# Performance work log

Measured on AMD Instinct MI355X. Metric: run time of the kernel, lower is better.

The kernel has to match this reference:

```python
import math
import jax, jax.numpy as jnp
import numpy as np

N_LAYERS = 2
D = 256        # d_input
N = 32         # d_state
BATCH = 8
L = 2048
SPK = 2


def setup_inputs() -> dict:
    key = jax.random.key(0)
    ks = jax.random.split(key, 20)
    def rn(i, shape, s=1.0):
        return jax.random.normal(ks[i], shape, jnp.float32) * s
    w = 0.02  # weight init scale
    lo, hi = math.log(1e-3), math.log(1e-1)
    return dict(
        x=rn(0, (BATCH, D, L)),
        ln_g=jnp.ones((N_LAYERS, 2, D), jnp.float32),
        ln_b=jnp.zeros((N_LAYERS, 2, D), jnp.float32),
        log_dt=lo + jax.random.uniform(ks[1], (N_LAYERS, D), jnp.float32) * (hi - lo),
        A_log_re=rn(2, (N_LAYERS, D, N), 0.5),
        A_im=rn(3, (N_LAYERS, D, N)) * math.pi,
        B_re=rn(4, (N_LAYERS, D, N), 0.5),
        B_im=rn(5, (N_LAYERS, D, N), 0.5),
        C_re=rn(6, (N_LAYERS, D, N), 0.5),
        C_im=rn(7, (N_LAYERS, D, N), 0.5),
        Dp=rn(8, (N_LAYERS, D)),
        s4o_W=rn(9, (N_LAYERS, D, D), w), s4o_b=jnp.zeros((N_LAYERS, D), jnp.float32),
        lin1_W=rn(10, (N_LAYERS, D, D), w), lin1_b=jnp.zeros((N_LAYERS, D), jnp.float32),
        lin2_W=rn(11, (N_LAYERS, D, D), w), lin2_b=jnp.zeros((N_LAYERS, D), jnp.float32),
        out_W0=rn(12, (D, D), w), out_b0=jnp.zeros((D,), jnp.float32),
        proj_W0=rn(13, (D, D), w), proj_b0=jnp.zeros((D,), jnp.float32),
        out_W1=rn(14, (D, SPK * D), w), out_b1=jnp.zeros((SPK * D,), jnp.float32),
        proj_W1=rn(15, (D, SPK * D), w), proj_b1=jnp.zeros((SPK * D,), jnp.float32),
    )


def _layernorm(x, g, b, eps=1e-5):
    m = jnp.mean(x, axis=-1, keepdims=True)
    v = jnp.var(x, axis=-1, keepdims=True)
    return (x - m) * jax.lax.rsqrt(v + eps) * g + b


def _s4(u, log_dt, A_log_re, A_im, B_re, B_im, C_re, C_im, Dp, oW, ob):
    # u: [B, L, H]. Diagonal SSM (ZOH discretization) -> global FFT convolution.
    Lq = u.shape[1]
    dt = jnp.exp(log_dt)                       # [H]
    A = -jnp.exp(A_log_re) + 1j * A_im         # [H, N], Re(A) < 0 for stability
    dtA = dt[:, None] * A                      # [H, N]
    dB = (B_re + 1j * B_im) * (jnp.exp(dtA) - 1.0) / A
    CB = (C_re + 1j * C_im) * dB               # [H, N]
    steps = jnp.arange(Lq)
    # Vandermonde kernel K[h, l] = 2 Re sum_n CB[h,n] * exp(dtA[h,n] * l)
    K = 2.0 * jnp.einsum('hn,hnl->hl', CB, jnp.exp(dtA[:, :, None] * steps)).real
    n = 2 * Lq  # linear (non-circular) convolution
    Uf = jnp.fft.rfft(u, n=n, axis=1)          # [B, nf, H]
    Kf = jnp.fft.rfft(K, n=n, axis=-1)         # [H, nf]
    y = jnp.fft.irfft(Uf * Kf.T[None], n=n, axis=1)[:, :Lq]
    y = y + u * Dp                              # skip connection D*u
    y = jax.nn.gelu(y, approximate=False)       # S4 activation='gelu'
    return y @ oW + ob                          # output_linear (postact='id')


def reference(x, ln_g, ln_b, log_dt, A_log_re, A_im, B_re, B_im, C_re, C_im, Dp,
              s4o_W, s4o_b, lin1_W, lin1_b, lin2_W, lin2_b,
              out_W0, out_b0, proj_W0, proj_b0, out_W1, out_b1, proj_W1, proj_b1):
    o = jnp.moveaxis(x, -1, -2)  # [B, L, D]
    heads = [(out_W0, out_b0, proj_W0, proj_b0), (out_W1, out_b1, proj_W1, proj_b1)]
    for i in range(N_LAYERS):
        oW, ob, pW, pb = heads[i]
        u = o
        o1 = _layernorm(u, ln_g[i, 0], ln_b[i, 0])
        o1 = _s4(o1, log_dt[i], A_log_re[i], A_im[i], B_re[i], B_im[i],
                 C_re[i], C_im[i], Dp[i], s4o_W[i], s4o_b[i])
        o1 = o1 @ lin1_W[i] + lin1_b[i] + u     # residual add
        o2 = _layernorm(o1, ln_g[i, 1], ln_b[i, 1])
        o2 = jax.nn.gelu(o2 @ lin2_W[i] + lin2_b[i], approximate=False)
        o = o2 @ oW + ob + (o1 @ pW + pb)
    o = jax.nn.relu(o)                          # output_activation
    Bsz, Lq, C = o.shape
    d = C // SPK
    o = jnp.moveaxis(o, -1, 0).reshape(SPK, d, Bsz, Lq)
    return jnp.moveaxis(o, 1, -2)               # [num_spks, B, d_input, L]
```

## Files before the change

kernel.cpp:

```cpp
#include <hip/hip_runtime.h>


#define BSZ 8
#define DM 256
#define LSEQ 2048
#define NST 32
#define TC 64
#define NCH 32
#define TOK (BSZ*LSEQ)
#define NL 2

typedef __attribute__((ext_vector_type(8))) short bf16x8;
typedef __attribute__((ext_vector_type(4))) float f32x4;
typedef unsigned short ushort_t;

__device__ __forceinline__ float b2f(unsigned short v) {
    unsigned int u = ((unsigned int)v) << 16;
    float f;
    __builtin_memcpy(&f, &u, 4);
    return f;
}
__device__ __forceinline__ unsigned short f2b(float f) {
    unsigned int u;
    __builtin_memcpy(&u, &f, 4);
    unsigned int r = (u + 0x7FFFu + ((u >> 16) & 1u)) >> 16;
    return (unsigned short)r;
}
__device__ __forceinline__ float gelu_f(float z) {
    float x = z * 0.70710678118654752f;
    float ax = fabsf(x);
    float t = 1.0f / (1.0f + 0.3275911f * ax);
    float poly = t * (0.254829592f + t * (-0.284496736f + t * (1.421413741f +
                 t * (-1.453152027f + t * 1.061405429f))));
    float erfax = 1.0f - poly * expf(-ax * ax);
    float er = (x < 0.0f) ? -erfax : erfax;
    return 0.5f * z * (1.0f + er);
}

__global__ void k_setup_modes(const float* log_dt, const float* Alr, const float* Aim,
                              const float* Bre, const float* Bim,
                              const float* Cre, const float* Cim,
                              float2* dtA, float2* lam, float2* lamT, float2* CB) {
    int idx = blockIdx.x * blockDim.x + threadIdx.x;
    if (idx >= NL * DM * NST) return;
    int h = (idx >> 5) & (DM - 1);
    int i = idx >> 13;
    float dt  = expf(log_dt[i * DM + h]);
    float Are = -expf(Alr[idx]);
    float Ai  = Aim[idx];
    float dr = dt * Are, di = dt * Ai;
    float er = expf(dr);
    float lr = er * cosf(di), li = er * sinf(di);
    float inv = 1.0f / (Are * Are + Ai * Ai);
    float e1r = lr - 1.0f, e1i = li;
    float tr = (e1r * Are + e1i * Ai) * inv;
    float ti = (e1i * Are - e1r * Ai) * inv;
    float br = Bre[idx], bi = Bim[idx];
    float dBr = br * tr - bi * ti, dBi = br * ti + bi * tr;
    float cr = Cre[idx], ci = Cim[idx];
    dtA[idx] = make_float2(dr, di);
    lam[idx] = make_float2(lr, li);
    CB[idx]  = make_float2(cr * dBr - ci * dBi, cr * dBi + ci * dBr);
    float pr = lr, pi = li;
    for (int s = 0; s < 6; ++s) { float nr = pr * pr - pi * pi; pi = 2.f * pr * pi; pr = nr; }
    lamT[idx] = make_float2(pr, pi);
}

__global__ void k_wcvt(const float* src, ushort_t* dst, int N) {
    int idx = blockIdx.x * 256 + threadIdx.x;
    if (idx >= N * 256) return;
    int n = idx >> 8, k = idx & 255;
    dst[idx] = f2b(src[(size_t)k * N + n]);
}

__global__ void k_wc_fuse(const float* Wa, const float* Wb, ushort_t* WBc) {
    int c = blockIdx.x;
    int r = threadIdx.x;
    const float* ar = Wa + (size_t)r * 256;
    float s = 0.f;
    for (int k = 0; k < 256; ++k) s = fmaf(ar[k], Wb[(size_t)k * 256 + c], s);
    WBc[(size_t)c * 256 + r] = f2b(s);
}
__global__ void k_bc_fuse(const float* s4ob, const float* Wb, const float* lin1b,
                          float* bc) {
    int c = threadIdx.x;
    float s = lin1b[c];
    for (int k = 0; k < 256; ++k) s = fmaf(s4ob[k], Wb[(size_t)k * 256 + c], s);
    bc[c] = s;
}

__global__ void k_setup_wk(const float2* dtA_l, const float2* lam_l, const float2* CB_l,
                           float* Ktab, float2* Wtab) {
    int idx = blockIdx.x * blockDim.x + threadIdx.x;
    if (idx >= DM * TC) return;
    int t = idx & (TC - 1);
    int h = idx >> 6;
    int base = h * NST;
    float ft = (float)t;
    float Ks = 0.f;
    for (int n = 0; n < NST; ++n) {
        float2 d = dtA_l[base + n]; float2 l1 = lam_l[base + n]; float2 cb = CB_l[base + n];
        float er = expf(d.x * ft);
        float cs = cosf(d.y * ft), sn = sinf(d.y * ft);
        float ltr = er * cs, lti = er * sn;
        Ks += cb.x * ltr - cb.y * lti;
        float p1r = ltr * l1.x - lti * l1.y, p1i = ltr * l1.y + lti * l1.x;
        Wtab[(h * NST + n) * TC + t] =
            make_float2(cb.x * p1r - cb.y * p1i, cb.x * p1i + cb.y * p1r);
    }
    Ktab[idx] = 2.f * Ks;
}

__global__ void k_transpose_in(const float* x, ushort_t* o) {
    __shared__ float tile[32][33];
    int b = blockIdx.z;
    int l0 = blockIdx.x * 32, d0 = blockIdx.y * 32;
    int tx = threadIdx.x, ty = threadIdx.y;
    for (int k = 0; k < 4; ++k)
        tile[ty + 8 * k][tx] = x[((size_t)b * DM + d0 + ty + 8 * k) * LSEQ + l0 + tx];
    __syncthreads();
    for (int k = 0; k < 4; ++k)
        o[((size_t)b * LSEQ + l0 + ty + 8 * k) * DM + d0 + tx] = f2b(tile[tx][ty + 8 * k]);
}

__global__ void k_layernorm(const ushort_t* src, ushort_t* dst,
                            const float* g, const float* bb) {
    __shared__ float r1[DM];
    __shared__ float r2[DM];
    int tok = blockIdx.x;
    int d = threadIdx.x;
    float v = b2f(src[(size_t)tok * DM + d]);
    r1[d] = v;
    r2[d] = v * v;
    __syncthreads();
    for (int s = DM / 2; s > 0; s >>= 1) {
        if (d < s) { r1[d] += r1[d + s]; r2[d] += r2[d + s]; }
        __syncthreads();
    }
    float m = r1[0] * (1.0f / DM);
    float var = r2[0] * (1.0f / DM) - m * m;
    float inv = rsqrtf(var + 1e-5f);
    dst[(size_t)tok * DM + d] = f2b((v - m) * inv * g[d] + bb[d]);
}

__global__ void k_layernorm_T(const ushort_t* src, ushort_t* dstT,
                              const float* g, const float* bb) {
    __shared__ float r1[DM];
    __shared__ float r2[DM];
    int tok = blockIdx.x;
    int d = threadIdx.x;
    float v = b2f(src[(size_t)tok * DM + d]);
    r1[d] = v;
    r2[d] = v * v;
    __syncthreads();
    for (int s = DM / 2; s > 0; s >>= 1) {
        if (d < s) { r1[d] += r1[d + s]; r2[d] += r2[d + s]; }
        __syncthreads();
    }
    float m = r1[0] * (1.0f / DM);
    float var = r2[0] * (1.0f / DM) - m * m;
    float inv = rsqrtf(var + 1e-5f);
    int b = tok >> 11, l = tok & 2047;
    dstT[((size_t)b * DM + d) * LSEQ + l] = f2b((v - m) * inv * g[d] + bb[d]);
}

__global__ void k_chunk_states(const ushort_t* uT, const float2* lam_l, float2* P) {
    int n = threadIdx.x & 31, hs = threadIdx.x >> 5;
    int c = blockIdx.x, h = blockIdx.y * 8 + hs, b = blockIdx.z;
    float2 lm = lam_l[h * NST + n];
    float sr = 0.f, si = 0.f;
    const ushort_t* up = uT + ((size_t)b * DM + h) * LSEQ + c * TC;
#pragma unroll 8
    for (int t = 0; t < TC; ++t) {
        float u = b2f(up[t]);
        float nr = fmaf(lm.x, sr, fmaf(-lm.y, si, u));
        float ni = fmaf(lm.x, si, lm.y * sr);
        sr = nr; si = ni;
    }
    P[(((size_t)b * DM + h) * NCH + c) * NST + n] = make_float2(sr, si);
}

__global__ void k_chunk_scan(const float2* lamT_l, float2* P) {
    int idx = blockIdx.x * blockDim.x + threadIdx.x;
    if (idx >= BSZ * DM * NST) return;
    int n = idx & 31, h = (idx >> 5) & 255, b = idx >> 13;
    float2 lT = lamT_l[h * NST + n];
    float hr = 0.f, hi = 0.f;
    float2* base = P + (((size_t)b * DM + h) * NCH) * NST + n;
    for (int c = 0; c < NCH; ++c) {
        float2 p = base[(size_t)c * NST];
        base[(size_t)c * NST] = make_float2(hr, hi);
        float nr = fmaf(lT.x, hr, fmaf(-lT.y, hi, p.x));
        float ni = fmaf(lT.x, hi, fmaf(lT.y, hr, p.y));
        hr = nr; hi = ni;
    }
}

__global__ void k_conv_out(const ushort_t* uT, ushort_t* G, const float* Ktab,
                           const float2* Wtab, const float2* S, const float* Dp_l) {
    int h = blockIdx.y;
    int tid = threadIdx.x;
    __shared__ float Kch[TC];
    __shared__ float Wre[NST][TC];
    __shared__ float Wim[NST][TC];
    __shared__ float uch[BSZ][TC + 1];
    __shared__ float hre[BSZ][NST + 1];
    __shared__ float him[BSZ][NST + 1];
    if (tid < TC) Kch[tid] = Ktab[h * TC + tid];
    for (int idx = tid; idx < NST * TC; idx += 128) {
        float2 wv = Wtab[(size_t)h * NST * TC + idx];
        Wre[idx >> 6][idx & 63] = wv.x;
        Wim[idx >> 6][idx & 63] = wv.y;
    }
    float dp = Dp_l[h];
    int b = tid >> 4, q = tid & 15, t0 = q * 4;
    for (int cc = 0; cc < 4; ++cc) {
        int c = blockIdx.x * 4 + cc;
        __syncthreads();
        for (int idx = tid; idx < BSZ * TC; idx += 128) {
            int bb = idx >> 6, t = idx & 63;
            uch[bb][t] = b2f(uT[((size_t)bb * DM + h) * LSEQ + c * TC + t]);
        }
        for (int idx = tid; idx < BSZ * NST; idx += 128) {
            int bb = idx >> 5, n = idx & 31;
            float2 hv = S[(((size_t)bb * DM + h) * NCH + c) * NST + n];
            hre[bb][n] = hv.x;
            him[bb][n] = hv.y;
        }
        __syncthreads();
        float s0 = 0, s1 = 0, s2 = 0, s3 = 0;
        float u0 = uch[b][t0], u1 = uch[b][t0 + 1], u2 = uch[b][t0 + 2], u3 = uch[b][t0 + 3];
        for (int d = 0; d <= t0; ++d) {
            float kk = Kch[d];
            s0 = fmaf(kk, u0, s0); s1 = fmaf(kk, u1, s1);
            s2 = fmaf(kk, u2, s2); s3 = fmaf(kk, u3, s3);
            u3 = u2; u2 = u1; u1 = u0;
            u0 = (d < t0) ? uch[b][t0 - d - 1] : 0.f;
        }
        {
            float k1 = Kch[t0 + 1], k2 = Kch[t0 + 2], k3 = Kch[t0 + 3];
            s1 = fmaf(k1, u1, s1); s2 = fmaf(k1, u2, s2); s3 = fmaf(k1, u3, s3);
            s2 = fmaf(k2, u1, s2); s3 = fmaf(k2, u2, s3);
            s3 = fmaf(k3, u1, s3);
        }
        float y0 = 0, y1 = 0, y2 = 0, y3 = 0;
#pragma unroll
        for (int n = 0; n < NST; ++n) {
            float hr = hre[b][n], hi = him[b][n];
            y0 += Wre[n][t0] * hr - Wim[n][t0] * hi;
            y1 += Wre[n][t0 + 1] * hr - Wim[n][t0 + 1] * hi;
            y2 += Wre[n][t0 + 2] * hr - Wim[n][t0 + 2] * hi;
            y3 += Wre[n][t0 + 3] * hr - Wim[n][t0 + 3] * hi;
        }
        size_t obase = ((size_t)b * LSEQ + c * TC + t0) * DM + h;
        float z;
        z = s0 + 2.f * y0 + dp * uch[b][t0];     G[obase]          = f2b(gelu_f(z));
        z = s1 + 2.f * y1 + dp * uch[b][t0 + 1]; G[obase + DM]     = f2b(gelu_f(z));
        z = s2 + 2.f * y2 + dp * uch[b][t0 + 2]; G[obase + 2 * DM] = f2b(gelu_f(z));
        z = s3 + 2.f * y3 + dp * uch[b][t0 + 3]; G[obase + 3 * DM] = f2b(gelu_f(z));
    }
}

__device__ __forceinline__ void stage_tile(const ushort_t* src, int row0,
                                           ushort_t (*dst)[256], int tid) {
    for (int idx = tid; idx < 64 * 32; idx += 256) {
        int r = idx >> 5, ch = (idx & 31) * 8;
        bf16x8 v = *(const bf16x8*)(src + (size_t)(row0 + r) * 256 + ch);
        *(bf16x8*)(&dst[r][ch ^ ((r & 7) << 3)]) = v;
    }
}
__device__ __forceinline__ void mma_tile(const ushort_t (*As)[256],
                                         const ushort_t (*Bs)[256],
                                         int wv, int l, f32x4* acc) {
    int lr = l & 15, lk = (l >> 4) * 8;
    int ax = (lr & 7) << 3;
#pragma unroll
    for (int k0 = 0; k0 < 256; k0 += 32) {
        bf16x8 a  = *(const bf16x8*)(&As[wv * 16 + lr][(lk + k0) ^ ax]);
        bf16x8 b0 = *(const bf16x8*)(&Bs[lr]          [(lk + k0) ^ ax]);
        bf16x8 b1 = *(const bf16x8*)(&Bs[16 + lr]     [(lk + k0) ^ ax]);
        bf16x8 b2 = *(const bf16x8*)(&Bs[32 + lr]     [(lk + k0) ^ ax]);
        bf16x8 b3 = *(const bf16x8*)(&Bs[48 + lr]     [(lk + k0) ^ ax]);
        acc[0] = __builtin_amdgcn_mfma_f32_16x16x32_bf16(a, b0, acc[0], 0, 0, 0);
        acc[1] = __builtin_amdgcn_mfma_f32_16x16x32_bf16(a, b1, acc[1], 0, 0, 0);
        acc[2] = __builtin_amdgcn_mfma_f32_16x16x32_bf16(a, b2, acc[2], 0, 0, 0);
        acc[3] = __builtin_amdgcn_mfma_f32_16x16x32_bf16(a, b3, acc[3], 0, 0, 0);
    }
}

__global__ void k_gemm_mfma(const ushort_t* A, const ushort_t* WBt,
                            const float* bias, const ushort_t* res,
                            ushort_t* C, int N, int flags) {
    __shared__ ushort_t As[64][256];
    __shared__ ushort_t Bs[64][256];
    int m0 = blockIdx.x * 64, n0 = blockIdx.y * 64;
    int tid = threadIdx.x;
    int wv = tid >> 6, l = tid & 63;
    stage_tile(A, m0, As, tid);
    stage_tile(WBt, n0, Bs, tid);
    __syncthreads();
    f32x4 acc[4] = {{0,0,0,0},{0,0,0,0},{0,0,0,0},{0,0,0,0}};
    mma_tile(As, Bs, wv, l, acc);
    int em = m0 + wv * 16 + (l >> 4) * 4;
    int en = n0 + (l & 15);
#pragma unroll
    for (int nt = 0; nt < 4; ++nt) {
        int n = en + nt * 16;
        float bsv = bias[n];
#pragma unroll
        for (int r = 0; r < 4; ++r) {
            int m = em + r;
            float v = acc[nt][r] + bsv;
            if (res) v += b2f(res[(size_t)m * DM + n]);
            if (flags & 1) v = gelu_f(v);
            if (flags & 8) v = fmaxf(v, 0.0f);
            C[(size_t)m * N + n] = f2b(v);
        }
    }
}

__global__ void k_gemm2_mfma(const ushort_t* Aa, const ushort_t* WBa,
                             const ushort_t* Ab, const ushort_t* WBb,
                             const float* biasA, const float* biasB,
                             ushort_t* C, int N, int flags) {
    __shared__ ushort_t As[64][256];
    __shared__ ushort_t Bs[64][256];
    int m0 = blockIdx.x * 64, n0 = blockIdx.y * 64;
    int tid = threadIdx.x;
    int wv = tid >> 6, l = tid & 63;
    f32x4 acc[4] = {{0,0,0,0},{0,0,0,0},{0,0,0,0},{0,0,0,0}};
    stage_tile(Aa, m0, As, tid);
    stage_tile(WBa, n0, Bs, tid);
    __syncthreads();
    mma_tile(As, Bs, wv, l, acc);
    __syncthreads();
    stage_tile(Ab, m0, As, tid);
    stage_tile(WBb, n0, Bs, tid);
    __syncthreads();
    mma_tile(As, Bs, wv, l, acc);
    int em = m0 + wv * 16 + (l >> 4) * 4;
    int en = n0 + (l & 15);
#pragma unroll
    for (int nt = 0; nt < 4; ++nt) {
        int n = en + nt * 16;
        float bsv = biasA[n] + biasB[n];
#pragma unroll
        for (int r = 0; r < 4; ++r) {
            int m = em + r;
            float v = acc[nt][r] + bsv;
            if (flags & 8) v = fmaxf(v, 0.0f);
            C[(size_t)m * N + n] = f2b(v);
        }
    }
}

__global__ void k_final_out(const ushort_t* F, float* out) {
    __shared__ float tile[32][33];
    int b = blockIdx.z;
    int l0 = blockIdx.x * 32, c0 = blockIdx.y * 32;
    int tx = threadIdx.x, ty = threadIdx.y;
    for (int k = 0; k < 4; ++k)
        tile[ty + 8 * k][tx] = b2f(F[((size_t)(b * LSEQ + l0 + ty + 8 * k)) * 512 + c0 + tx]);
    __syncthreads();
    for (int k = 0; k < 4; ++k) {
        int cg = c0 + ty + 8 * k;
        int s = cg >> 8, cc = cg & 255;
        out[(((size_t)s * BSZ + b) * DM + cc) * LSEQ + l0 + tx] = tile[tx][ty + 8 * k];
    }
}

extern "C" void kernel_launch(void* const* d_in, const int* in_sizes, int n_in,
                              void* d_out, int out_size, void* d_ws, size_t ws_size,
                              hipStream_t stream) {
    (void)in_sizes; (void)n_in; (void)out_size;
    float* out = (float*)d_out;

    const float* x      = (const float*)d_in[0];
    const float* ln_g   = (const float*)d_in[1];
    const float* ln_b   = (const float*)d_in[2];
    const float* log_dt = (const float*)d_in[3];
    const float* Alr    = (const float*)d_in[4];
    const float* Aim    = (const float*)d_in[5];
    const float* Bre    = (const float*)d_in[6];
    const float* Bim    = (const float*)d_in[7];
    const float* Cre    = (const float*)d_in[8];
    const float* Cim    = (const float*)d_in[9];
    const float* Dp     = (const float*)d_in[10];
    const float* s4oW   = (const float*)d_in[11];
    const float* s4ob   = (const float*)d_in[12];
    const float* lin1W  = (const float*)d_in[13];
    const float* lin1b  = (const float*)d_in[14];
    const float* lin2W  = (const float*)d_in[15];
    const float* lin2b  = (const float*)d_in[16];
    const float* headW[2] = {(const float*)d_in[17], (const float*)d_in[21]};
    const float* headb[2] = {(const float*)d_in[18], (const float*)d_in[22]};
    const float* projW[2] = {(const float*)d_in[19], (const float*)d_in[23]};
    const float* projb[2] = {(const float*)d_in[20], (const float*)d_in[24]};

    char* w = (char*)d_ws;
    ushort_t* A0 = (ushort_t*)w;  w += (size_t)TOK * DM * 2;
    ushort_t* A1 = (ushort_t*)w;  w += (size_t)TOK * DM * 2;
    ushort_t* A2 = (ushort_t*)w;  w += (size_t)TOK * DM * 2;
    float2* dtA  = (float2*)w;    w += (size_t)NL * DM * NST * 8;
    float2* lam  = (float2*)w;    w += (size_t)NL * DM * NST * 8;
    float2* lamT = (float2*)w;    w += (size_t)NL * DM * NST * 8;
    float2* CB   = (float2*)w;    w += (size_t)NL * DM * NST * 8;
    float2* P    = (float2*)w;    w += (size_t)BSZ * DM * NCH * NST * 8;
    float2* Wtab = (float2*)w;    w += (size_t)DM * NST * TC * 8;
    float*  KtabC = (float*)w;    w += (size_t)DM * TC * 4;
    ushort_t* wb = (ushort_t*)w;  w += (size_t)655360 * 2;
    float*  bc   = (float*)w;     w += 512 * 4;
    if ((size_t)(w - (char*)d_ws) > ws_size) return;
    ushort_t* F = (ushort_t*)P;

    ushort_t* WB_lin2[2] = {wb + 0,      wb + 65536};
    ushort_t* WB_head0   = wb + 131072;
    ushort_t* WB_proj0   = wb + 196608;
    ushort_t* WB_head1   = wb + 262144;
    ushort_t* WB_proj1   = wb + 393216;
    ushort_t* WBc[2]     = {wb + 524288, wb + 589824};

    k_setup_modes<<<NL * DM * NST / 256, 256, 0, stream>>>(
        log_dt, Alr, Aim, Bre, Bim, Cre, Cim, dtA, lam, lamT, CB);
    for (int i = 0; i < NL; ++i) {
        size_t wf = (size_t)i * DM * DM;
        k_wcvt<<<256, 256, 0, stream>>>(lin2W + wf, WB_lin2[i], DM);
        k_wc_fuse<<<256, 256, 0, stream>>>(s4oW + wf, lin1W + wf, WBc[i]);
        k_bc_fuse<<<1, 256, 0, stream>>>(s4ob + i * DM, lin1W + wf, lin1b + i * DM,
                                         bc + i * 256);
    }
    k_wcvt<<<256, 256, 0, stream>>>(headW[0], WB_head0, DM);
    k_wcvt<<<256, 256, 0, stream>>>(projW[0], WB_proj0, DM);
    k_wcvt<<<512, 256, 0, stream>>>(headW[1], WB_head1, 2 * DM);
    k_wcvt<<<512, 256, 0, stream>>>(projW[1], WB_proj1, 2 * DM);
    {
        dim3 gt(LSEQ / 32, DM / 32, BSZ);
        dim3 bt(32, 8);
        k_transpose_in<<<gt, bt, 0, stream>>>(x, A0);
    }

    dim3 gg(TOK / 64, DM / 64);
    for (int i = 0; i < NL; ++i) {
        ushort_t* U = (i == 0) ? A0 : A2;
        ushort_t* T = (i == 0) ? A1 : A0;
        ushort_t* G = (i == 0) ? A2 : A1;
        size_t off = (size_t)i * DM * NST;

        k_layernorm_T<<<TOK, DM, 0, stream>>>(U, T, ln_g + (2 * i) * DM,
                                              ln_b + (2 * i) * DM);
        k_setup_wk<<<DM * TC / 128, 128, 0, stream>>>(dtA + off, lam + off,
                                                      CB + off, KtabC, Wtab);
        {
            dim3 gs(NCH, DM / 8, BSZ);
            k_chunk_states<<<gs, 256, 0, stream>>>(T, lam + off, P);
        }
        k_chunk_scan<<<BSZ * DM * NST / 256, 256, 0, stream>>>(lamT + off, P);
        {
            dim3 gc(NCH / 4, DM);
            k_conv_out<<<gc, 128, 0, stream>>>(T, G, KtabC, Wtab, P, Dp + i * DM);
        }
        k_gemm_mfma<<<gg, 256, 0, stream>>>(G, WBc[i], bc + i * 256, U, T, DM, 0);
        k_layernorm<<<TOK, DM, 0, stream>>>(T, G, ln_g + (2 * i + 1) * DM,
                                            ln_b + (2 * i + 1) * DM);
        k_gemm_mfma<<<gg, 256, 0, stream>>>(G, WB_lin2[i], lin2b + i * DM, 0, U, DM, 1);
        if (i == 0) {
            k_gemm2_mfma<<<gg, 256, 0, stream>>>(U, WB_head0, T, WB_proj0,
                                                 headb[0], projb[0], A2, DM, 0);
        } else {
            dim3 gh(TOK / 64, 2 * DM / 64);
            k_gemm2_mfma<<<gh, 256, 0, stream>>>(U, WB_head1, T, WB_proj1,
                                                 headb[1], projb[1], F, 2 * DM, 8);
        }
    }
    {
        dim3 gf(LSEQ / 32, 2 * DM / 32, BSZ);
        dim3 bf(32, 8);
        k_final_out<<<gf, bf, 0, stream>>>(F, out);
    }
}
```

Baseline: 504.7 us.

## Recast intra-chunk convolution and state output as one bf16 MFMA GEMM per channel

Replaces the scalar FMA kernel for intra-chunk causal convolution plus state-to-output projection with a per-channel MFMA GEMM. A 64x128 matrix is built from the Toeplitz kernel and the 2x-scaled real/imag output weights, and it multiplies a 256x128 operand made of u chunks and chunk-start states across all batch and chunk pairs. This moves the work onto matrix cores and cuts the launch to 256 blocks. In exchange, the kernel and states are rounded to bf16, which may cost accuracy, and the grid is small.

```diff
diff --git a/kernel.cpp b/kernel.cpp
--- a/kernel.cpp
+++ b/kernel.cpp
@@ -196,68 +196,68 @@
     }
 }
 
-__global__ void k_conv_out(const ushort_t* uT, ushort_t* G, const float* Ktab,
-                           const float2* Wtab, const float2* S, const float* Dp_l) {
-    int h = blockIdx.y;
+__global__ void k_conv_mfma(const ushort_t* uT, ushort_t* G, const float* Ktab,
+                            const float2* Wtab, const float2* P, const float* Dp_l) {
+    __shared__ ushort_t As[64][128];
+    __shared__ ushort_t Bs[256][128];
+    int h = blockIdx.x;
     int tid = threadIdx.x;
-    __shared__ float Kch[TC];
-    __shared__ float Wre[NST][TC];
-    __shared__ float Wim[NST][TC];
-    __shared__ float uch[BSZ][TC + 1];
-    __shared__ float hre[BSZ][NST + 1];
-    __shared__ float him[BSZ][NST + 1];
-    if (tid < TC) Kch[tid] = Ktab[h * TC + tid];
-    for (int idx = tid; idx < NST * TC; idx += 128) {
-        float2 wv = Wtab[(size_t)h * NST * TC + idx];
-        Wre[idx >> 6][idx & 63] = wv.x;
-        Wim[idx >> 6][idx & 63] = wv.y;
+    int wv = tid >> 6, l = tid & 63;
+    for (int idx = tid; idx < 64 * 128; idx += 256) {
+        int r = idx >> 7, e = idx & 127;
+        float v;
+        if (e < 64) {
+            int d = r - e;
+            v = (d >= 0) ? Ktab[h * TC + d] : 0.f;
+        } else {
+            int j = e - 64;
+            float2 wc = Wtab[((size_t)h * NST + (j >> 1)) * TC + r];
+            v = (j & 1) ? -2.f * wc.y : 2.f * wc.x;
+        }
+        As[r][e ^ ((r & 7) << 3)] = f2b(v);
+    }
+    for (int idx = tid; idx < 256 * 8; idx += 256) {
+        int row = idx >> 3, ch = (idx & 7) * 8;
+        int b = row >> 5, c = row & 31;
+        bf16x8 v = *(const bf16x8*)(uT + ((size_t)b * DM + h) * LSEQ + c * TC + ch);
+        *(bf16x8*)(&Bs[row][ch ^ ((row & 7) << 3)]) = v;
+    }
+    for (int idx = tid; idx < 256 * 32; idx += 256) {
+        int row = idx >> 5, n = idx & 31;
+        int b = row >> 5, c = row & 31;
+        float2 s = P[(((size_t)b * DM + h) * NCH + c) * NST + n];
+        int x = (row & 7) << 3;
+        Bs[row][(64 + 2 * n) ^ x]     = f2b(s.x);
+        Bs[row][(64 + 2 * n + 1) ^ x] = f2b(s.y);
+    }
+    __syncthreads();
+    int lr = l & 15, lk = (l >> 4) * 8;
+    int ax = (lr & 7) << 3;
+    f32x4 acc[16];
+#pragma unroll
+    for (int i = 0; i < 16; ++i) acc[i] = (f32x4){0.f, 0.f, 0.f, 0.f};
+#pragma unroll
+    for (int k0 = 0; k0 < 128; k0 += 32) {
+        bf16x8 a = *(const bf16x8*)(&As[wv * 16 + lr][(lk + k0) ^ ax]);
+#pragma unroll
+        for (int nt = 0; nt < 16; ++nt) {
+            bf16x8 b = *(const bf16x8*)(&Bs[nt * 16 + lr][(lk + k0) ^ ax]);
+            acc[nt] = __builtin_amdgcn_mfma_f32_16x16x32_bf16(a, b, acc[nt], 0, 0, 0);
+        }
     }
     float dp = Dp_l[h];
-    int b = tid >> 4, q = tid & 15, t0 = q * 4;
-    for (int cc = 0; cc < 4; ++cc) {
-        int c = blockIdx.x * 4 + cc;
-        __syncthreads();
-        for (int idx = tid; idx < BSZ * TC; idx += 128) {
-            int bb = idx >> 6, t = idx & 63;
-            uch[bb][t] = b2f(uT[((size_t)bb * DM + h) * LSEQ + c * TC + t]);
-        }
-        for (int idx = tid; idx < BSZ * NST; idx += 128) {
-            int bb = idx >> 5, n = idx & 31;
-            float2 hv = S[(((size_t)bb * DM + h) * NCH + c) * NST + n];
-            hre[bb][n] = hv.x;
-            him[bb][n] = hv.y;
-        }
-        __syncthreads();
-        float s0 = 0, s1 = 0, s2 = 0, s3 = 0;
-        float u0 = uch[b][t0], u1 = uch[b][t0 + 1], u2 = uch[b][t0 + 2], u3 = uch[b][t0 + 3];
-        for (int d = 0; d <= t0; ++d) {
-            float kk = Kch[d];
-            s0 = fmaf(kk, u0, s0); s1 = fmaf(kk, u1, s1);
-            s2 = fmaf(kk, u2, s2); s3 = fmaf(kk, u3, s3);
-            u3 = u2; u2 = u1; u1 = u0;
-            u0 = (d < t0) ? uch[b][t0 - d - 1] : 0.f;
-        }
-        {
-            float k1 = Kch[t0 + 1], k2 = Kch[t0 + 2], k3 = Kch[t0 + 3];
-            s1 = fmaf(k1, u1, s1); s2 = fmaf(k1, u2, s2); s3 = fmaf(k1, u3, s3);
-            s2 = fmaf(k2, u1, s2); s3 = fmaf(k2, u2, s3);
-            s3 = fmaf(k3, u1, s3);
-        }
-        float y0 = 0, y1 = 0, y2 = 0, y3 = 0;
-#pragma unroll
-        for (int n = 0; n < NST; ++n) {
-            float hr = hre[b][n], hi = him[b][n];
-            y0 += Wre[n][t0] * hr - Wim[n][t0] * hi;
-            y1 += Wre[n][t0 + 1] * hr - Wim[n][t0 + 1] * hi;
-            y2 += Wre[n][t0 + 2] * hr - Wim[n][t0 + 2] * hi;
-            y3 += Wre[n][t0 + 3] * hr - Wim[n][t0 + 3] * hi;
-        }
-        size_t obase = ((size_t)b * LSEQ + c * TC + t0) * DM + h;
-        float z;
-        z = s0 + 2.f * y0 + dp * uch[b][t0];     G[obase]          = f2b(gelu_f(z));
-        z = s1 + 2.f * y1 + dp * uch[b][t0 + 1]; G[obase + DM]     = f2b(gelu_f(z));
-        z = s2 + 2.f * y2 + dp * uch[b][t0 + 2]; G[obase + 2 * DM] = f2b(gelu_f(z));
-        z = s3 + 2.f * y3 + dp * uch[b][t0 + 3]; G[obase + 3 * DM] = f2b(gelu_f(z));
+#pragma unroll
+    for (int nt = 0; nt < 16; ++nt) {
+        int bc = nt * 16 + (l & 15);
+        int b = bc >> 5, c = bc & 31;
+        int bx = (bc & 7) << 3;
+#pragma unroll
+        for (int r = 0; r < 4; ++r) {
+            int t = wv * 16 + (l >> 4) * 4 + r;
+            float uv = b2f(Bs[bc][t ^ bx]);
+            float z = acc[nt][r] + dp * uv;
+            G[((size_t)b * LSEQ + c * TC + t) * DM + h] = f2b(gelu_f(z));
+        }
     }
 }
 
@@ -455,10 +455,7 @@
             k_chunk_states<<<gs, 256, 0, stream>>>(T, lam + off, P);
         }
         k_chunk_scan<<<BSZ * DM * NST / 256, 256, 0, stream>>>(lamT + off, P);
-        {
-            dim3 gc(NCH / 4, DM);
-            k_conv_out<<<gc, 128, 0, stream>>>(T, G, KtabC, Wtab, P, Dp + i * DM);
-        }
+        k_conv_mfma<<<DM, 256, 0, stream>>>(T, G, KtabC, Wtab, P, Dp + i * DM);
         k_gemm_mfma<<<gg, 256, 0, stream>>>(G, WBc[i], bc + i * 256, U, T, DM, 0);
         k_layernorm<<<TOK, DM, 0, stream>>>(T, G, ln_g + (2 * i + 1) * DM,
                                             ln_b + (2 * i + 1) * DM);
```

Result: faster. 458.0 us (-9.2%).
